# Kernel optimization log

Measured on AMD Instinct MI355X. Metric: run time of the kernel, lower is better.

Reference implementation:

```python
import jax, jax.numpy as jnp
import numpy as np
import math

EMBED_DIM = 512
NUM_HEADS = 8
BLOCK_SIZE = 16
RANK = 32
B, N = 1, 4096
HEAD_DIM = EMBED_DIM // NUM_HEADS
SCALE = math.sqrt(HEAD_DIM)  # note: the torch module MULTIPLIES q by sqrt(head_dim)


def _block_causal_mask(n, block):
    # block-diagonal lower-triangular mask, identical for every head
    idx = jnp.arange(n)
    same_block = (idx[:, None] // block) == (idx[None, :] // block)
    causal = idx[:, None] >= idx[None, :]
    return (same_block & causal).astype(jnp.float32)  # [N, N]


def setup_inputs() -> dict:
    key = jax.random.key(0)
    ks = jax.random.split(key, 12)
    s = 0.02
    C, R = EMBED_DIM, RANK
    return {
        "x": jax.random.normal(ks[0], (B, N, C), dtype=jnp.float32),
        # low-rank query proj: Linear(C->R) then Linear(R->C); torch weight is [out, in]
        "q_w1": jax.random.normal(ks[1], (R, C), dtype=jnp.float32) * s,
        "q_w2": jax.random.normal(ks[2], (C, R), dtype=jnp.float32) * s,
        # key_value: Linear(C->2R) then Linear(2R->2C)
        "kv_w1": jax.random.normal(ks[3], (2 * R, C), dtype=jnp.float32) * s,
        "kv_w2": jax.random.normal(ks[4], (2 * C, 2 * R), dtype=jnp.float32) * s,
        # dynamic_focus: depthwise 1x1 conv (per-channel scale+bias) then pointwise 1x1 conv
        "dw_w": jax.random.normal(ks[5], (C,), dtype=jnp.float32) * s,
        "dw_b": jax.random.normal(ks[6], (C,), dtype=jnp.float32) * s,
        "pw_w": jax.random.normal(ks[7], (C, C), dtype=jnp.float32) * s,
        "pw_b": jax.random.normal(ks[8], (C,), dtype=jnp.float32) * s,
        # output proj: Linear(C->R) then Linear(R->C)
        "p_w1": jax.random.normal(ks[9], (R, C), dtype=jnp.float32) * s,
        "p_w2": jax.random.normal(ks[10], (C, R), dtype=jnp.float32) * s,
    }


def reference(x, q_w1, q_w2, kv_w1, kv_w2, dw_w, dw_b, pw_w, pw_b, p_w1, p_w2):
    Bv, Nv, C = x.shape
    H, D = NUM_HEADS, HEAD_DIM

    # low-rank q / kv projections (no bias)
    q = (x @ q_w1.T) @ q_w2.T                              # [B, N, C]
    kv = (x @ kv_w1.T) @ kv_w2.T                           # [B, N, 2C]

    q = q.reshape(Bv, Nv, H, D).transpose(0, 2, 1, 3)      # [B, H, N, D]
    kv = kv.reshape(Bv, Nv, 2, H, D).transpose(2, 0, 3, 1, 4)
    k, v = kv[0], kv[1]                                    # [B, H, N, D]

    q = q * SCALE
    attn = jnp.einsum("bhnd,bhmd->bhnm", q, k)             # [B, H, N, N]
    # faithful to source: full-row softmax FIRST, then block-diag causal mask
    mask = _block_causal_mask(Nv, BLOCK_SIZE)              # [N, N]
    attn = jax.nn.softmax(attn, axis=-1) * mask

    wv = jnp.einsum("bhnm,bhmd->bhnd", attn, v)            # [B, H, N, D]
    wv = wv.transpose(0, 2, 1, 3).reshape(Bv, Nv, C)       # [B, N, C]

    # dynamic_focus: depthwise 1x1 conv == per-channel affine; pointwise 1x1 conv == linear.
    # Spatial reshape to (sqrt(N), sqrt(N)) is a no-op for 1x1 convs, so stay in [B, N, C].
    dyn = wv * dw_w + dw_b
    dyn = dyn @ pw_w.T + pw_b

    y = dyn + x
    y = (y @ p_w1.T) @ p_w2.T
    return y
```

## Files before the change

kernel.cpp:

```cpp
#include <hip/hip_runtime.h>

#define NFULL 4096
#define CDIM  512
#define HEADS 8
#define DDIM  64

typedef unsigned short u16;
typedef short bf16x8 __attribute__((ext_vector_type(8)));
typedef float f32x4 __attribute__((ext_vector_type(4)));

#if __has_builtin(__builtin_amdgcn_exp2f)
__device__ __forceinline__ float exp2_hw(float x) { return __builtin_amdgcn_exp2f(x); }
#else
__device__ __forceinline__ float exp2_hw(float x) {
  float r;
  asm volatile("v_exp_f32 %0, %1\n\ts_nop 1" : "=v"(r) : "v"(x));
  return r;
}
#endif
#define EXP2(x) exp2_hw(x)

#define QSCALE 11.541560327111707f

__device__ __forceinline__ float dot4(float4 a, float4 b) {
  return a.x * b.x + a.y * b.y + a.z * b.z + a.w * b.w;
}

__device__ __forceinline__ u16 f2bf(float x) {
  union { float f; unsigned u; } v; v.f = x;
  unsigned r = v.u + 0x7fffu + ((v.u >> 16) & 1u);
  return (u16)(r >> 16);
}

__device__ __forceinline__ float bf2f(u16 b) {
  union { unsigned u; float f; } v; v.u = ((unsigned)b) << 16;
  return v.f;
}

__global__ __launch_bounds__(256) void k_pre(const float* __restrict__ x,
                                             const float* __restrict__ qw1,
                                             const float* __restrict__ kvw1,
                                             u16* __restrict__ t_bf,
                                             const float* __restrict__ pww,
                                             const float* __restrict__ dww,
                                             const float* __restrict__ dwb,
                                             const float* __restrict__ pwb,
                                             const float* __restrict__ pw1,
                                             const float* __restrict__ pw2,
                                             float* __restrict__ bias2,
                                             u16* __restrict__ pwbf,
                                             u16* __restrict__ pw1bf,
                                             u16* __restrict__ pw2bf) {
  __shared__ __align__(16) u16 Xs[32][72];
  __shared__ __align__(16) u16 Ws[96][72];
  const int tid = threadIdx.x;

  if (blockIdx.x >= 128) {
    const int b = blockIdx.x - 128;
    if (b < 2) {
      const int c = b * 256 + tid;
      float acc = 0.f;
      for (int e = 0; e < 512; e += 4)
        acc += dot4(*(const float4*)&pww[(size_t)c * 512 + e], *(const float4*)&dwb[e]);
      bias2[c] = acc + pwb[c];
    } else {
      const float* src;
      u16* dst;
      bool scale = false;
      int base;
      if (b < 66)      { base = (b - 2) * 4096 + tid * 16;  src = pww; dst = pwbf; scale = true; }
      else if (b < 70) { base = (b - 66) * 4096 + tid * 16; src = pw1; dst = pw1bf; }
      else             { base = (b - 70) * 4096 + tid * 16; src = pw2; dst = pw2bf; }
      const int e0 = base & 511;
      u16 o[16];
#pragma unroll
      for (int q = 0; q < 4; ++q) {
        float4 w = *(const float4*)&src[base + q * 4];
        if (scale) {
          const float4 d = *(const float4*)&dww[e0 + q * 4];
          w.x *= d.x; w.y *= d.y; w.z *= d.z; w.w *= d.w;
        }
        o[q * 4 + 0] = f2bf(w.x); o[q * 4 + 1] = f2bf(w.y);
        o[q * 4 + 2] = f2bf(w.z); o[q * 4 + 3] = f2bf(w.w);
      }
      *(uint4*)&dst[base] = *(const uint4*)&o[0];
      *(uint4*)&dst[base + 8] = *(const uint4*)&o[8];
    }
    return;
  }

  const int r0 = blockIdx.x * 32;
  const int wave = tid >> 6, lane = tid & 63;
  const int lrow = lane & 15, g = lane >> 4;
  const int rs = wave >> 1, ws2 = wave & 1;

  f32x4 acc[3];
#pragma unroll
  for (int sub = 0; sub < 3; ++sub) acc[sub] = (f32x4){0.f, 0.f, 0.f, 0.f};

  for (int k0 = 0; k0 < 512; k0 += 64) {
    __syncthreads();
    {
      const int row = tid >> 3, c16 = (tid & 7) * 8;
      const float* __restrict__ src = x + (size_t)(r0 + row) * 512 + k0 + c16;
      const float4 v0 = *(const float4*)(src);
      const float4 v1 = *(const float4*)(src + 4);
      u16 tmp[8] = {f2bf(v0.x), f2bf(v0.y), f2bf(v0.z), f2bf(v0.w),
                    f2bf(v1.x), f2bf(v1.y), f2bf(v1.z), f2bf(v1.w)};
      *(uint4*)&Xs[row][c16] = *(const uint4*)&tmp[0];
    }
    for (int u = tid; u < 768; u += 256) {
      const int c = u >> 3, c16 = (u & 7) * 8;
      const float* __restrict__ src =
          (c < 32 ? qw1 + (size_t)c * 512 : kvw1 + (size_t)(c - 32) * 512) + k0 + c16;
      const float4 v0 = *(const float4*)(src);
      const float4 v1 = *(const float4*)(src + 4);
      u16 tmp[8] = {f2bf(v0.x), f2bf(v0.y), f2bf(v0.z), f2bf(v0.w),
                    f2bf(v1.x), f2bf(v1.y), f2bf(v1.z), f2bf(v1.w)};
      *(uint4*)&Ws[c][c16] = *(const uint4*)&tmp[0];
    }
    __syncthreads();
    const bf16x8 a0 = *(const bf16x8*)&Xs[rs * 16 + lrow][g * 8];
    const bf16x8 a1 = *(const bf16x8*)&Xs[rs * 16 + lrow][32 + g * 8];
#pragma unroll
    for (int sub = 0; sub < 3; ++sub) {
      const int c = (ws2 * 3 + sub) * 16 + lrow;
      const bf16x8 b0 = *(const bf16x8*)&Ws[c][g * 8];
      const bf16x8 b1 = *(const bf16x8*)&Ws[c][32 + g * 8];
      acc[sub] = __builtin_amdgcn_mfma_f32_16x16x32_bf16(a0, b0, acc[sub], 0, 0, 0);
      acc[sub] = __builtin_amdgcn_mfma_f32_16x16x32_bf16(a1, b1, acc[sub], 0, 0, 0);
    }
  }
#pragma unroll
  for (int sub = 0; sub < 3; ++sub)
#pragma unroll
    for (int j = 0; j < 4; ++j)
      t_bf[(size_t)(r0 + rs * 16 + g * 4 + j) * 96 + (ws2 * 3 + sub) * 16 + lrow] =
          f2bf(acc[sub][j]);
}

__global__ __launch_bounds__(256) void k_proj2(const u16* __restrict__ t_bf,
                                               const float* __restrict__ qw2,
                                               const float* __restrict__ kvw2,
                                               u16* __restrict__ qb,
                                               u16* __restrict__ kb,
                                               float* __restrict__ vh) {
  __shared__ __align__(16) u16 Ts[64][72];
  __shared__ __align__(16) u16 Wsh[128][72];
  const int cb = blockIdx.x % 12;
  const int r0 = (blockIdx.x / 12) * 64;
  const int tid = threadIdx.x;
  const int wave = tid >> 6, lane = tid & 63;
  const int lrow = lane & 15, g = lane >> 4;
  const bool isq = cb < 4;
  const int c0 = isq ? cb * 128 : 512 + (cb - 4) * 128;

  for (int u = tid; u < 512; u += 256) {
    const int row = u >> 3, ch = (u & 7) * 8;
    uint4 v = {0u, 0u, 0u, 0u};
    if (isq) {
      if (ch < 32) v = *(const uint4*)&t_bf[(size_t)(r0 + row) * 96 + ch];
    } else {
      v = *(const uint4*)&t_bf[(size_t)(r0 + row) * 96 + 32 + ch];
    }
    *(uint4*)&Ts[row][ch] = v;
  }
  if (isq) {
    for (int u = tid; u < 1024; u += 256) {
      const int col = u >> 3, cf = (u & 7) * 4;
      const float4 v = *(const float4*)&qw2[(size_t)(c0 + col) * 32 + cf];
      u16 tmp[4] = {f2bf(v.x), f2bf(v.y), f2bf(v.z), f2bf(v.w)};
      *(uint2*)&Wsh[col][cf] = *(const uint2*)&tmp[0];
    }
  } else {
    for (int u = tid; u < 2048; u += 256) {
      const int col = u >> 4, cf = (u & 15) * 4;
      const float4 v = *(const float4*)&kvw2[(size_t)(c0 - 512 + col) * 64 + cf];
      u16 tmp[4] = {f2bf(v.x), f2bf(v.y), f2bf(v.z), f2bf(v.w)};
      *(uint2*)&Wsh[col][cf] = *(const uint2*)&tmp[0];
    }
  }
  __syncthreads();

  if (isq) {
    const bf16x8 aq = *(const bf16x8*)&Ts[wave * 16 + lrow][g * 8];
#pragma unroll
    for (int sub = 0; sub < 8; ++sub) {
      const bf16x8 b0 = *(const bf16x8*)&Wsh[sub * 16 + lrow][g * 8];
      f32x4 acc = {0.f, 0.f, 0.f, 0.f};
      acc = __builtin_amdgcn_mfma_f32_16x16x32_bf16(aq, b0, acc, 0, 0, 0);
      const int colg = c0 + sub * 16 + lrow;
#pragma unroll
      for (int j = 0; j < 4; ++j) {
        const int n = r0 + wave * 16 + g * 4 + j;
        qb[((size_t)(colg >> 6) * NFULL + n) * 64 + (colg & 63)] = f2bf(acc[j] * QSCALE);
      }
    }
  } else {
    const bf16x8 a0 = *(const bf16x8*)&Ts[wave * 16 + lrow][g * 8];
    const bf16x8 a1 = *(const bf16x8*)&Ts[wave * 16 + lrow][32 + g * 8];
#pragma unroll
    for (int sub = 0; sub < 8; ++sub) {
      const bf16x8 b0 = *(const bf16x8*)&Wsh[sub * 16 + lrow][g * 8];
      const bf16x8 b1 = *(const bf16x8*)&Wsh[sub * 16 + lrow][32 + g * 8];
      f32x4 acc = {0.f, 0.f, 0.f, 0.f};
      acc = __builtin_amdgcn_mfma_f32_16x16x32_bf16(a0, b0, acc, 0, 0, 0);
      acc = __builtin_amdgcn_mfma_f32_16x16x32_bf16(a1, b1, acc, 0, 0, 0);
      const int colg = c0 + sub * 16 + lrow;
#pragma unroll
      for (int j = 0; j < 4; ++j) {
        const int n = r0 + wave * 16 + g * 4 + j;
        if (colg < 1024) {
          const int c2 = colg - 512;
          kb[((size_t)(c2 >> 6) * NFULL + n) * 64 + (c2 & 63)] = f2bf(acc[j]);
        } else {
          const int c2 = colg - 1024;
          vh[((size_t)(c2 >> 6) * NFULL + n) * 64 + (c2 & 63)] = acc[j];
        }
      }
    }
  }
}

__global__ __launch_bounds__(256, 4) void k_attn(const u16* __restrict__ qb,
                                                 const u16* __restrict__ kb,
                                                 const float* __restrict__ vh,
                                                 u16* __restrict__ wv16,
                                                 float* __restrict__ dsp) {
  __shared__ __align__(16) u16 KB[4][64][64];
  __shared__ float P_lds[4][16][17];
  __shared__ float Ds[4][4][16];

  const int h = blockIdx.x & 7;
  const int qt = (blockIdx.x >> 3) & 63;
  const int s = blockIdx.x >> 9;
  const int q0 = qt * 64;
  const int tid = threadIdx.x;
  const int wave = tid >> 6, lane = tid & 63;
  const int lrow = lane & 15, g = lane >> 4;

  const u16* __restrict__ Qg = qb + ((size_t)h * NFULL + q0) * 64;
  const u16* __restrict__ Kg = kb + ((size_t)h * NFULL + (size_t)s * 2048) * 64;

  bf16x8 qf[4][2];
#pragma unroll
  for (int f = 0; f < 4; ++f) {
    qf[f][0] = *(const bf16x8*)&Qg[(f * 16 + lrow) * 64 + g * 8];
    qf[f][1] = *(const bf16x8*)&Qg[(f * 16 + lrow) * 64 + 32 + g * 8];
  }

  const int srow8 = lane >> 3;
  const int scol = ((lane & 7) ^ srow8) << 3;

#define STAGE(T, B)                                                           \
  do {                                                                        \
    const u16* tb_ = Kg + (size_t)(T) * 64 * 64;                              \
    {                                                                         \
      const u16* src_ = tb_ + (wave * 16 + srow8) * 64 + scol;                \
      u16* dst_ = &KB[(B)][wave * 16][0];                                     \
      __builtin_amdgcn_global_load_lds(                                       \
          (const __attribute__((address_space(1))) unsigned*)src_,            \
          (__attribute__((address_space(3))) unsigned*)dst_, 16, 0, 0);       \
    }                                                                         \
    {                                                                         \
      const u16* src_ = tb_ + (wave * 16 + 8 + srow8) * 64 + scol;            \
      u16* dst_ = &KB[(B)][wave * 16][0] + 512;                               \
      __builtin_amdgcn_global_load_lds(                                       \
          (const __attribute__((address_space(1))) unsigned*)src_,            \
          (__attribute__((address_space(3))) unsigned*)dst_, 16, 0, 0);       \
    }                                                                         \
  } while (0)

  const int rsw = wave * 16 + lrow;
  const int x0 = (g ^ (lrow & 7)) * 8;
  const int x1 = ((g + 4) ^ (lrow & 7)) * 8;

  float dsum[4] = {0.f, 0.f, 0.f, 0.f};
  const bool dg = (s == (qt >> 5));
  const int tdiag = qt & 31;

  auto tile = [&](int t, int b) {
    const bf16x8 kf0 = *(const bf16x8*)&KB[b][rsw][x0];
    const bf16x8 kf1 = *(const bf16x8*)&KB[b][rsw][x1];
    f32x4 a[4];
    __builtin_amdgcn_s_setprio(1);
#pragma unroll
    for (int f = 0; f < 4; ++f) {
      f32x4 t4 = {0.f, 0.f, 0.f, 0.f};
      t4 = __builtin_amdgcn_mfma_f32_16x16x32_bf16(kf0, qf[f][0], t4, 0, 0, 0);
      t4 = __builtin_amdgcn_mfma_f32_16x16x32_bf16(kf1, qf[f][1], t4, 0, 0, 0);
      a[f] = t4;
    }
    __builtin_amdgcn_s_setprio(0);
    const bool isd = dg && (t == tdiag);
#pragma unroll
    for (int f = 0; f < 4; ++f) {
      const float e0 = EXP2(a[f][0]);
      const float e1 = EXP2(a[f][1]);
      const float e2 = EXP2(a[f][2]);
      const float e3 = EXP2(a[f][3]);
      dsum[f] += (e0 + e1) + (e2 + e3);
      if (isd && f == wave) {
        const int rr = g * 4;
        P_lds[wave][rr + 0][lrow] = (rr + 0 <= lrow) ? e0 : 0.f;
        P_lds[wave][rr + 1][lrow] = (rr + 1 <= lrow) ? e1 : 0.f;
        P_lds[wave][rr + 2][lrow] = (rr + 2 <= lrow) ? e2 : 0.f;
        P_lds[wave][rr + 3][lrow] = (rr + 3 <= lrow) ? e3 : 0.f;
      }
    }
  };

  STAGE(0, 0); STAGE(1, 1); STAGE(2, 2);

  for (int t = 0; t < 28; t += 2) {
    STAGE(t + 3, (t + 3) & 3);
    asm volatile("s_waitcnt vmcnt(6)" ::: "memory");
    tile(t, t & 3);
    STAGE(t + 4, (t + 4) & 3);
    asm volatile("s_waitcnt vmcnt(6)" ::: "memory");
    tile(t + 1, (t + 1) & 3);
  }
  STAGE(31, 3);
  asm volatile("s_waitcnt vmcnt(6)" ::: "memory");
  tile(28, 0);
  asm volatile("s_waitcnt vmcnt(4)" ::: "memory");
  tile(29, 1);
  asm volatile("s_waitcnt vmcnt(2)" ::: "memory");
  tile(30, 2);
  asm volatile("s_waitcnt vmcnt(0)" ::: "memory");
  tile(31, 3);
#undef STAGE

#pragma unroll
  for (int f = 0; f < 4; ++f) {
    dsum[f] += __shfl_xor(dsum[f], 16);
    dsum[f] += __shfl_xor(dsum[f], 32);
  }
  if (g == 0) {
#pragma unroll
    for (int f = 0; f < 4; ++f) Ds[wave][f][lrow] = dsum[f];
  }
  __syncthreads();

  if (tid < 64) {
    const int f = tid >> 4, r = tid & 15;
    const float den = Ds[0][f][r] + Ds[1][f][r] + Ds[2][f][r] + Ds[3][f][r];
    dsp[((size_t)s * HEADS + h) * NFULL + q0 + f * 16 + r] = den;
  }

  if (dg) {
    const float* __restrict__ V =
        vh + ((size_t)h * NFULL + q0 + wave * 16) * 64 + g * 16;
    float o[16];
#pragma unroll
    for (int dd = 0; dd < 16; ++dd) o[dd] = 0.f;
#pragma unroll
    for (int k = 0; k < 16; ++k) {
      const float p = P_lds[wave][k][lrow];
      const float4 v0 = *(const float4*)&V[k * 64 + 0];
      const float4 v1 = *(const float4*)&V[k * 64 + 4];
      const float4 v2 = *(const float4*)&V[k * 64 + 8];
      const float4 v3 = *(const float4*)&V[k * 64 + 12];
      o[0] += p * v0.x;  o[1] += p * v0.y;  o[2] += p * v0.z;  o[3] += p * v0.w;
      o[4] += p * v1.x;  o[5] += p * v1.y;  o[6] += p * v1.z;  o[7] += p * v1.w;
      o[8] += p * v2.x;  o[9] += p * v2.y;  o[10] += p * v2.z; o[11] += p * v2.w;
      o[12] += p * v3.x; o[13] += p * v3.y; o[14] += p * v3.z; o[15] += p * v3.w;
    }
    u16 ob[16];
#pragma unroll
    for (int dd = 0; dd < 16; ++dd) ob[dd] = f2bf(o[dd]);
    u16* __restrict__ op =
        wv16 + (size_t)(q0 + wave * 16 + lrow) * CDIM + h * 64 + g * 16;
    *(uint4*)&op[0] = *(const uint4*)&ob[0];
    *(uint4*)&op[8] = *(const uint4*)&ob[8];
  }
}

__global__ __launch_bounds__(256) void k_dyn(const u16* __restrict__ wv16,
                                             const float* __restrict__ x,
                                             const u16* __restrict__ pwbf,
                                             const float* __restrict__ bias2,
                                             const float* __restrict__ dsp,
                                             u16* __restrict__ y16) {
  __shared__ __align__(16) u16 Ab[64][72];
  __shared__ __align__(16) u16 Wb[64][72];
  const int rb = blockIdx.x >> 3, cb = blockIdx.x & 7;
  const int r0 = rb * 64, c0 = cb * 64;
  const int tid = threadIdx.x;
  const int wave = tid >> 6, lane = tid & 63;
  const int lrow = lane & 15, g = lane >> 4;
  const int srow = tid >> 2;
  const int skc = (tid & 3) * 16;

  float inv8[8];
#pragma unroll
  for (int hh = 0; hh < 8; ++hh) {
    const size_t base = (size_t)hh * NFULL + r0 + srow;
    inv8[hh] = 1.0f / (dsp[base] + dsp[(size_t)8 * NFULL + base]);
  }

  f32x4 acc[4];
#pragma unroll
  for (int ct = 0; ct < 4; ++ct) acc[ct] = (f32x4){0.f, 0.f, 0.f, 0.f};

  const u16* __restrict__ ap = wv16 + (size_t)(r0 + srow) * 512 + skc;
  const u16* __restrict__ wp = pwbf + (size_t)(c0 + srow) * 512 + skc;
  uint4 av0 = *(const uint4*)ap;
  uint4 av1 = *(const uint4*)(ap + 8);
  uint4 w0 = *(const uint4*)wp;
  uint4 w1 = *(const uint4*)(wp + 8);

  for (int k0 = 0; k0 < 512; k0 += 64) {
    const float sc = inv8[k0 >> 6];
    u16 ab16[16];
    const u16* pa0 = (const u16*)&av0;
    const u16* pa1 = (const u16*)&av1;
#pragma unroll
    for (int e = 0; e < 8; ++e) ab16[e] = f2bf(bf2f(pa0[e]) * sc);
#pragma unroll
    for (int e = 0; e < 8; ++e) ab16[8 + e] = f2bf(bf2f(pa1[e]) * sc);
    __syncthreads();
    *(uint4*)&Ab[srow][skc] = *(const uint4*)&ab16[0];
    *(uint4*)&Ab[srow][skc + 8] = *(const uint4*)&ab16[8];
    *(uint4*)&Wb[srow][skc] = w0;
    *(uint4*)&Wb[srow][skc + 8] = w1;
    __syncthreads();
    if (k0 + 64 < 512) {
      av0 = *(const uint4*)(ap + k0 + 64);
      av1 = *(const uint4*)(ap + k0 + 64 + 8);
      w0 = *(const uint4*)(wp + k0 + 64);
      w1 = *(const uint4*)(wp + k0 + 64 + 8);
    }
#pragma unroll
    for (int kk = 0; kk < 2; ++kk) {
      const bf16x8 af = *(const bf16x8*)&Ab[wave * 16 + lrow][kk * 32 + g * 8];
#pragma unroll
      for (int ct = 0; ct < 4; ++ct) {
        const bf16x8 wf = *(const bf16x8*)&Wb[ct * 16 + lrow][kk * 32 + g * 8];
        acc[ct] = __builtin_amdgcn_mfma_f32_16x16x32_bf16(wf, af, acc[ct], 0, 0, 0);
      }
    }
  }
  const int row = r0 + wave * 16 + lrow;
#pragma unroll
  for (int ct = 0; ct < 4; ++ct) {
    const int c = c0 + ct * 16 + g * 4;
    const float4 bb = *(const float4*)&bias2[c];
    const float4 xv = *(const float4*)&x[(size_t)row * 512 + c];
    u16 o4[4];
    o4[0] = f2bf(acc[ct][0] + bb.x + xv.x);
    o4[1] = f2bf(acc[ct][1] + bb.y + xv.y);
    o4[2] = f2bf(acc[ct][2] + bb.z + xv.z);
    o4[3] = f2bf(acc[ct][3] + bb.w + xv.w);
    *(uint2*)&y16[(size_t)row * 512 + c] = *(const uint2*)o4;
  }
}

__global__ __launch_bounds__(256) void k_pout(const u16* __restrict__ y16,
                                              const u16* __restrict__ pw1bf,
                                              const u16* __restrict__ pw2bf,
                                              float* __restrict__ out) {
  __shared__ __align__(16) u16 yb[16][520];
  __shared__ float tp_part[2][32][17];
  const int r0 = blockIdx.x * 16;
  const int tid = threadIdx.x;
  const int wave = tid >> 6, lane = tid & 63;
  const int lrow = lane & 15, g = lane >> 4;

  for (int rep = 0; rep < 4; ++rep) {
    const int idx = rep * 256 + tid;
    const int row = idx >> 6, c8 = (idx & 63) * 8;
    *(uint4*)&yb[row][c8] = *(const uint4*)&y16[(size_t)(r0 + row) * 512 + c8];
  }
  __syncthreads();

  {
    const int ct1 = wave & 1, kh = wave >> 1;
    f32x4 acc = {0.f, 0.f, 0.f, 0.f};
#pragma unroll
    for (int ks = 0; ks < 8; ++ks) {
      const int K = kh * 256 + ks * 32 + g * 8;
      const bf16x8 aw = *(const bf16x8*)&pw1bf[(size_t)(ct1 * 16 + lrow) * 512 + K];
      const bf16x8 bf = *(const bf16x8*)&yb[lrow][K];
      acc = __builtin_amdgcn_mfma_f32_16x16x32_bf16(aw, bf, acc, 0, 0, 0);
    }
#pragma unroll
    for (int j = 0; j < 4; ++j)
      tp_part[kh][ct1 * 16 + g * 4 + j][lrow] = acc[j];
  }
  __syncthreads();

  union { u16 a[8]; bf16x8 v; } bq;
#pragma unroll
  for (int i = 0; i < 8; ++i) {
    const int k = g * 8 + i;
    bq.a[i] = f2bf(tp_part[0][k][lrow] + tp_part[1][k][lrow]);
  }

#pragma unroll
  for (int t = 0; t < 8; ++t) {
    const int ct = wave * 8 + t;
    const bf16x8 aw = *(const bf16x8*)&pw2bf[(size_t)(ct * 16 + lrow) * 32 + g * 8];
    f32x4 acc = {0.f, 0.f, 0.f, 0.f};
    acc = __builtin_amdgcn_mfma_f32_16x16x32_bf16(aw, bq.v, acc, 0, 0, 0);
    float4 res;
    res.x = acc[0]; res.y = acc[1]; res.z = acc[2]; res.w = acc[3];
    *(float4*)&out[(size_t)(r0 + lrow) * 512 + ct * 16 + g * 4] = res;
  }
}

extern "C" void kernel_launch(void* const* d_in, const int* in_sizes, int n_in,
                              void* d_out, int out_size, void* d_ws, size_t ws_size,
                              hipStream_t stream) {
  const float* x     = (const float*)d_in[0];
  const float* q_w1  = (const float*)d_in[1];
  const float* q_w2  = (const float*)d_in[2];
  const float* kv_w1 = (const float*)d_in[3];
  const float* kv_w2 = (const float*)d_in[4];
  const float* dw_w  = (const float*)d_in[5];
  const float* dw_b  = (const float*)d_in[6];
  const float* pw_w  = (const float*)d_in[7];
  const float* pw_b  = (const float*)d_in[8];
  const float* p_w1  = (const float*)d_in[9];
  const float* p_w2  = (const float*)d_in[10];
  float* out = (float*)d_out;

  char* ws = (char*)d_ws;
  float* dsp   = (float*)ws;
  float* bias2 = (float*)(ws + 262144);
  u16*   pwbf  = (u16*)(ws + 262144 + 4096);
  u16*   pw1bf = pwbf + 262144;
  u16*   pw2bf = pw1bf + 16384;
  u16*   t_bf  = pw2bf + 16384;
  u16*   qbw   = t_bf + (size_t)NFULL * 96;
  u16*   kbw   = qbw + (size_t)HEADS * NFULL * DDIM;
  float* vh    = (float*)(kbw + (size_t)HEADS * NFULL * DDIM);
  u16*   wv16  = (u16*)(vh + (size_t)HEADS * NFULL * DDIM);
  u16*   y16   = qbw;

  k_pre<<<202, 256, 0, stream>>>(x, q_w1, kv_w1, t_bf, pw_w, dw_w, dw_b, pw_b,
                                 p_w1, p_w2, bias2, pwbf, pw1bf, pw2bf);
  k_proj2<<<(NFULL / 64) * 12, 256, 0, stream>>>(t_bf, q_w2, kv_w2, qbw, kbw, vh);
  k_attn<<<2 * HEADS * (NFULL / 64), 256, 0, stream>>>(qbw, kbw, vh, wv16, dsp);
  k_dyn<<<(NFULL / 64) * 8, 256, 0, stream>>>(wv16, x, pwbf, bias2, dsp, y16);
  k_pout<<<NFULL / 16, 256, 0, stream>>>(y16, pw1bf, pw2bf, out);
}
```

Baseline: 83.33 us.

## Share staged K tiles across two query groups with 512-thread attention blocks

The attention kernel now uses 512-thread blocks covering 128 query rows, split into two 64-row groups that share each K tile staged into LDS. This halves the global-to-LDS K traffic per query row and the number of blocks. The staging loop now issues one load per wave and uses explicit barriers with waitcnt to synchronise the shared buffers. In exchange it adds per-tile block-wide barriers, and the launch-bounds change lowers the guaranteed blocks per CU and grid parallelism.

```diff
diff --git a/kernel.cpp b/kernel.cpp
--- a/kernel.cpp
+++ b/kernel.cpp
@@ -222,24 +222,26 @@
   }
 }
 
-__global__ __launch_bounds__(256, 4) void k_attn(const u16* __restrict__ qb,
+__global__ __launch_bounds__(512, 2) void k_attn(const u16* __restrict__ qb,
                                                  const u16* __restrict__ kb,
                                                  const float* __restrict__ vh,
                                                  u16* __restrict__ wv16,
                                                  float* __restrict__ dsp) {
   __shared__ __align__(16) u16 KB[4][64][64];
-  __shared__ float P_lds[4][16][17];
-  __shared__ float Ds[4][4][16];
+  __shared__ float P_lds[8][16][17];
+  __shared__ float Ds[4][8][16];
 
   const int h = blockIdx.x & 7;
-  const int qt = (blockIdx.x >> 3) & 63;
-  const int s = blockIdx.x >> 9;
-  const int q0 = qt * 64;
+  const int qb2 = (blockIdx.x >> 3) & 31;
+  const int s = blockIdx.x >> 8;
+  const int q0 = qb2 * 128;
   const int tid = threadIdx.x;
   const int wave = tid >> 6, lane = tid & 63;
   const int lrow = lane & 15, g = lane >> 4;
-
-  const u16* __restrict__ Qg = qb + ((size_t)h * NFULL + q0) * 64;
+  const int G = wave >> 2;
+  const int kw = wave & 3;
+
+  const u16* __restrict__ Qg = qb + ((size_t)h * NFULL + q0 + G * 64) * 64;
   const u16* __restrict__ Kg = kb + ((size_t)h * NFULL + (size_t)s * 2048) * 64;
 
   bf16x8 qf[4][2];
@@ -249,35 +251,26 @@
     qf[f][1] = *(const bf16x8*)&Qg[(f * 16 + lrow) * 64 + 32 + g * 8];
   }
 
-  const int srow8 = lane >> 3;
-  const int scol = ((lane & 7) ^ srow8) << 3;
+  const int srow = wave * 8 + (lane >> 3);
+  const int scol = ((lane & 7) ^ (lane >> 3)) << 3;
 
 #define STAGE(T, B)                                                           \
   do {                                                                        \
-    const u16* tb_ = Kg + (size_t)(T) * 64 * 64;                              \
-    {                                                                         \
-      const u16* src_ = tb_ + (wave * 16 + srow8) * 64 + scol;                \
-      u16* dst_ = &KB[(B)][wave * 16][0];                                     \
-      __builtin_amdgcn_global_load_lds(                                       \
-          (const __attribute__((address_space(1))) unsigned*)src_,            \
-          (__attribute__((address_space(3))) unsigned*)dst_, 16, 0, 0);       \
-    }                                                                         \
-    {                                                                         \
-      const u16* src_ = tb_ + (wave * 16 + 8 + srow8) * 64 + scol;            \
-      u16* dst_ = &KB[(B)][wave * 16][0] + 512;                               \
-      __builtin_amdgcn_global_load_lds(                                       \
-          (const __attribute__((address_space(1))) unsigned*)src_,            \
-          (__attribute__((address_space(3))) unsigned*)dst_, 16, 0, 0);       \
-    }                                                                         \
+    const u16* src_ = Kg + (size_t)(T) * 4096 + srow * 64 + scol;             \
+    u16* dst_ = &KB[(B)][wave * 8][0];                                        \
+    __builtin_amdgcn_global_load_lds(                                         \
+        (const __attribute__((address_space(1))) unsigned*)src_,              \
+        (__attribute__((address_space(3))) unsigned*)dst_, 16, 0, 0);         \
   } while (0)
 
-  const int rsw = wave * 16 + lrow;
+  const int rsw = kw * 16 + lrow;
   const int x0 = (g ^ (lrow & 7)) * 8;
   const int x1 = ((g + 4) ^ (lrow & 7)) * 8;
 
   float dsum[4] = {0.f, 0.f, 0.f, 0.f};
-  const bool dg = (s == (qt >> 5));
-  const int tdiag = qt & 31;
+  const bool dg = (s == (q0 >> 11));
+  const int J = G * 4 + kw;
+  const int tdiag = ((q0 >> 4) + J - s * 128) >> 2;
 
   auto tile = [&](int t, int b) {
     const bf16x8 kf0 = *(const bf16x8*)&KB[b][rsw][x0];
@@ -300,36 +293,42 @@
       const float e2 = EXP2(a[f][2]);
       const float e3 = EXP2(a[f][3]);
       dsum[f] += (e0 + e1) + (e2 + e3);
-      if (isd && f == wave) {
+      if (isd && f == kw) {
         const int rr = g * 4;
-        P_lds[wave][rr + 0][lrow] = (rr + 0 <= lrow) ? e0 : 0.f;
-        P_lds[wave][rr + 1][lrow] = (rr + 1 <= lrow) ? e1 : 0.f;
-        P_lds[wave][rr + 2][lrow] = (rr + 2 <= lrow) ? e2 : 0.f;
-        P_lds[wave][rr + 3][lrow] = (rr + 3 <= lrow) ? e3 : 0.f;
+        P_lds[J][rr + 0][lrow] = (rr + 0 <= lrow) ? e0 : 0.f;
+        P_lds[J][rr + 1][lrow] = (rr + 1 <= lrow) ? e1 : 0.f;
+        P_lds[J][rr + 2][lrow] = (rr + 2 <= lrow) ? e2 : 0.f;
+        P_lds[J][rr + 3][lrow] = (rr + 3 <= lrow) ? e3 : 0.f;
       }
     }
   };
 
+#define SYNC(N)                                                 \
+  asm volatile("s_waitcnt vmcnt(" #N ")" ::: "memory");         \
+  __builtin_amdgcn_s_barrier();                                 \
+  __builtin_amdgcn_sched_barrier(0)
+
   STAGE(0, 0); STAGE(1, 1); STAGE(2, 2);
 
   for (int t = 0; t < 28; t += 2) {
+    SYNC(2);
+    tile(t, t & 3);
     STAGE(t + 3, (t + 3) & 3);
-    asm volatile("s_waitcnt vmcnt(6)" ::: "memory");
-    tile(t, t & 3);
+    SYNC(2);
+    tile(t + 1, (t + 1) & 3);
     STAGE(t + 4, (t + 4) & 3);
-    asm volatile("s_waitcnt vmcnt(6)" ::: "memory");
-    tile(t + 1, (t + 1) & 3);
-  }
+  }
+  SYNC(2);
+  tile(28, 0);
   STAGE(31, 3);
-  asm volatile("s_waitcnt vmcnt(6)" ::: "memory");
-  tile(28, 0);
-  asm volatile("s_waitcnt vmcnt(4)" ::: "memory");
+  SYNC(2);
   tile(29, 1);
-  asm volatile("s_waitcnt vmcnt(2)" ::: "memory");
+  SYNC(1);
   tile(30, 2);
-  asm volatile("s_waitcnt vmcnt(0)" ::: "memory");
+  SYNC(0);
   tile(31, 3);
 #undef STAGE
+#undef SYNC
 
 #pragma unroll
   for (int f = 0; f < 4; ++f) {
@@ -338,25 +337,25 @@
   }
   if (g == 0) {
 #pragma unroll
-    for (int f = 0; f < 4; ++f) Ds[wave][f][lrow] = dsum[f];
+    for (int f = 0; f < 4; ++f) Ds[kw][G * 4 + f][lrow] = dsum[f];
   }
   __syncthreads();
 
-  if (tid < 64) {
-    const int f = tid >> 4, r = tid & 15;
-    const float den = Ds[0][f][r] + Ds[1][f][r] + Ds[2][f][r] + Ds[3][f][r];
-    dsp[((size_t)s * HEADS + h) * NFULL + q0 + f * 16 + r] = den;
+  if (tid < 128) {
+    const int J2 = tid >> 4, r = tid & 15;
+    const float den = Ds[0][J2][r] + Ds[1][J2][r] + Ds[2][J2][r] + Ds[3][J2][r];
+    dsp[((size_t)s * HEADS + h) * NFULL + q0 + J2 * 16 + r] = den;
   }
 
   if (dg) {
     const float* __restrict__ V =
-        vh + ((size_t)h * NFULL + q0 + wave * 16) * 64 + g * 16;
+        vh + ((size_t)h * NFULL + q0 + J * 16) * 64 + g * 16;
     float o[16];
 #pragma unroll
     for (int dd = 0; dd < 16; ++dd) o[dd] = 0.f;
 #pragma unroll
     for (int k = 0; k < 16; ++k) {
-      const float p = P_lds[wave][k][lrow];
+      const float p = P_lds[J][k][lrow];
       const float4 v0 = *(const float4*)&V[k * 64 + 0];
       const float4 v1 = *(const float4*)&V[k * 64 + 4];
       const float4 v2 = *(const float4*)&V[k * 64 + 8];
@@ -370,7 +369,7 @@
 #pragma unroll
     for (int dd = 0; dd < 16; ++dd) ob[dd] = f2bf(o[dd]);
     u16* __restrict__ op =
-        wv16 + (size_t)(q0 + wave * 16 + lrow) * CDIM + h * 64 + g * 16;
+        wv16 + (size_t)(q0 + J * 16 + lrow) * CDIM + h * 64 + g * 16;
     *(uint4*)&op[0] = *(const uint4*)&ob[0];
     *(uint4*)&op[8] = *(const uint4*)&ob[8];
   }
@@ -541,7 +540,7 @@
   k_pre<<<202, 256, 0, stream>>>(x, q_w1, kv_w1, t_bf, pw_w, dw_w, dw_b, pw_b,
                                  p_w1, p_w2, bias2, pwbf, pw1bf, pw2bf);
   k_proj2<<<(NFULL / 64) * 12, 256, 0, stream>>>(t_bf, q_w2, kv_w2, qbw, kbw, vh);
-  k_attn<<<2 * HEADS * (NFULL / 64), 256, 0, stream>>>(qbw, kbw, vh, wv16, dsp);
+  k_attn<<<2 * HEADS * (NFULL / 128), 512, 0, stream>>>(qbw, kbw, vh, wv16, dsp);
   k_dyn<<<(NFULL / 64) * 8, 256, 0, stream>>>(wv16, x, pwbf, bias2, dsp, y16);
   k_pout<<<NFULL / 16, 256, 0, stream>>>(y16, pw1bf, pw2bf, out);
 }
```

After: 91.78 us. 1.1x slower.
